# Kernel tuning notes

Hardware: AMD Instinct MI355X
Metric: run time of the kernel (lower is better)

## Reference

```python
import jax, jax.numpy as jnp
import numpy as np


def _bilinear_resample(imgs, dvfs):
    # imgs: (B,H,W,C), dvfs: (B,H,W,2) with channel 0 = x(width) offset, 1 = y(height) offset
    B, H, W, C = imgs.shape
    fx = jnp.arange(W, dtype=imgs.dtype)[None, None, :] + dvfs[..., 0]  # (B,H,W)
    fy = jnp.arange(H, dtype=imgs.dtype)[None, :, None] + dvfs[..., 1]  # (B,H,W)

    x0f = jnp.floor(fx)
    y0f = jnp.floor(fy)
    wx = fx - x0f  # fractional weights
    wy = fy - y0f
    x0 = x0f.astype(jnp.int32)
    y0 = y0f.astype(jnp.int32)
    x1 = x0 + 1
    y1 = y0 + 1

    def gather(iy, ix):
        # zero-padding semantics for out-of-bounds corners (tf resampler behavior)
        valid = (ix >= 0) & (ix < W) & (iy >= 0) & (iy < H)
        ixc = jnp.clip(ix, 0, W - 1)
        iyc = jnp.clip(iy, 0, H - 1)
        vals = jax.vmap(lambda im, yy, xx: im[yy, xx])(imgs, iyc, ixc)  # (B,H,W,C)
        return vals * valid[..., None].astype(imgs.dtype)

    v00 = gather(y0, x0)
    v01 = gather(y0, x1)
    v10 = gather(y1, x0)
    v11 = gather(y1, x1)

    wx = wx[..., None]
    wy = wy[..., None]
    return (v00 * (1 - wx) * (1 - wy)
            + v01 * wx * (1 - wy)
            + v10 * (1 - wx) * wy
            + v11 * wx * wy)


def setup_inputs() -> dict:
    key = jax.random.key(0)
    k1, k2 = jax.random.split(key)
    B, H, W = 32, 1024, 1024
    imgs = jax.random.normal(k1, (B, H, W, 1), dtype=jnp.float32)
    dvfs = jax.random.normal(k2, (B, H, W, 2), dtype=jnp.float32)
    return {"imgs": imgs, "dvfs": dvfs}


def reference(imgs, dvfs):
    return _bilinear_resample(imgs, dvfs)
```

## Files before the change

kernel.cpp:

```cpp
#include <hip/hip_runtime.h>


#define H_DIM 1024
#define W_DIM 1024
#define HW_SHIFT 20
#define HW_PIX (1 << HW_SHIFT)

__device__ __forceinline__ float gather_zp(const float* __restrict__ img,
                                           int yy, int xx) {
    bool valid = (xx >= 0) & (xx < W_DIM) & (yy >= 0) & (yy < H_DIM);
    int xc = min(max(xx, 0), W_DIM - 1);
    int yc = min(max(yy, 0), H_DIM - 1);
    float v = img[yc * W_DIM + xc];
    return valid ? v : 0.0f;
}

__global__ __launch_bounds__(256) void bilerp_kernel(
        const float* __restrict__ imgs,
        const float* __restrict__ dvfs,
        float* __restrict__ out,
        int total_pixels) {
    int pix = blockIdx.x * 256 + threadIdx.x;
    if (pix >= total_pixels) return;

    int b   = pix >> HW_SHIFT;
    int rem = pix & (HW_PIX - 1);
    int y   = rem >> 10;
    int x   = rem & (W_DIM - 1);

    const float* __restrict__ img = imgs + ((long long)b << HW_SHIFT);

    union { double d64; float2 f2; } cvt;
    cvt.d64 = __builtin_nontemporal_load(
        reinterpret_cast<const double*>(dvfs) + pix);
    float dx = cvt.f2.x;
    float dy = cvt.f2.y;

    float fx = (float)x + dx;
    float fy = (float)y + dy;
    float x0f = floorf(fx);
    float y0f = floorf(fy);
    float wx = fx - x0f;
    float wy = fy - y0f;
    int x0 = (int)x0f;
    int y0 = (int)y0f;

    float v00 = gather_zp(img, y0,     x0);
    float v01 = gather_zp(img, y0,     x0 + 1);
    float v10 = gather_zp(img, y0 + 1, x0);
    float v11 = gather_zp(img, y0 + 1, x0 + 1);

    float res = v00 * (1.0f - wx) * (1.0f - wy)
              + v01 * wx          * (1.0f - wy)
              + v10 * (1.0f - wx) * wy
              + v11 * wx          * wy;

    __builtin_nontemporal_store(res, out + pix);
}

extern "C" void kernel_launch(void* const* d_in, const int* in_sizes, int n_in,
                              void* d_out, int out_size, void* d_ws, size_t ws_size,
                              hipStream_t stream) {
    const float* imgs = (const float*)d_in[0];
    const float* dvfs = (const float*)d_in[1];
    float* out = (float*)d_out;

    int total_pixels = out_size;
    int block = 256;
    int grid = (total_pixels + block - 1) / block;

    bilerp_kernel<<<grid, block, 0, stream>>>(imgs, dvfs, out, total_pixels);
}
```

Before: 505.9 us.

## Stage image tiles with halo in shared memory for bilinear gathers

Each block now processes a 64x64 output tile per batch image, first loading a 81x81 halo region of the source image into LDS. Bilinear corner lookups read from LDS when the sampled point falls inside the halo, and fall back to global gathers otherwise. The aim is to replace scattered global/L2 gathers with LDS reads. In exchange it adds a synchronization barrier, about 1.6x redundant image loading because of the halo, and lower occupancy from the LDS footprint.

```diff
diff --git a/kernel.cpp b/kernel.cpp
--- a/kernel.cpp
+++ b/kernel.cpp
@@ -4,7 +4,9 @@
 #define H_DIM 1024
 #define W_DIM 1024
 #define HW_SHIFT 20
-#define HW_PIX (1 << HW_SHIFT)
+#define TILE 64
+#define HALO 8
+#define S_DIM (TILE + 2 * HALO + 1)
 
 __device__ __forceinline__ float gather_zp(const float* __restrict__ img,
                                            int yy, int xx) {
@@ -18,44 +20,81 @@
 __global__ __launch_bounds__(256) void bilerp_kernel(
         const float* __restrict__ imgs,
         const float* __restrict__ dvfs,
-        float* __restrict__ out,
-        int total_pixels) {
-    int pix = blockIdx.x * 256 + threadIdx.x;
-    if (pix >= total_pixels) return;
+        float* __restrict__ out) {
+    __shared__ float tile[S_DIM * S_DIM];
 
-    int b   = pix >> HW_SHIFT;
-    int rem = pix & (HW_PIX - 1);
-    int y   = rem >> 10;
-    int x   = rem & (W_DIM - 1);
+    const int gx0 = blockIdx.x * TILE;
+    const int gy0 = blockIdx.y * TILE;
+    const int b   = blockIdx.z;
+    const int tid = threadIdx.x;
 
     const float* __restrict__ img = imgs + ((long long)b << HW_SHIFT);
 
-    union { double d64; float2 f2; } cvt;
-    cvt.d64 = __builtin_nontemporal_load(
-        reinterpret_cast<const double*>(dvfs) + pix);
-    float dx = cvt.f2.x;
-    float dy = cvt.f2.y;
+    const int x_base = gx0 - HALO;
+    const int y_base = gy0 - HALO;
+    for (int idx = tid; idx < S_DIM * S_DIM; idx += 256) {
+        int r = idx / S_DIM;
+        int c = idx - r * S_DIM;
+        int gy = y_base + r;
+        int gx = x_base + c;
+        float v = 0.0f;
+        if ((unsigned)gy < (unsigned)H_DIM && (unsigned)gx < (unsigned)W_DIM)
+            v = img[(gy << 10) + gx];
+        tile[idx] = v;
+    }
+    __syncthreads();
 
-    float fx = (float)x + dx;
-    float fy = (float)y + dy;
-    float x0f = floorf(fx);
-    float y0f = floorf(fy);
-    float wx = fx - x0f;
-    float wy = fy - y0f;
-    int x0 = (int)x0f;
-    int y0 = (int)y0f;
+    const int tx = tid & 63;
+    const int ty = tid >> 6;
+    const float* __restrict__ dv_img =
+        dvfs + (((long long)b << HW_SHIFT) << 1);
+    float* __restrict__ out_img = out + ((long long)b << HW_SHIFT);
 
-    float v00 = gather_zp(img, y0,     x0);
-    float v01 = gather_zp(img, y0,     x0 + 1);
-    float v10 = gather_zp(img, y0 + 1, x0);
-    float v11 = gather_zp(img, y0 + 1, x0 + 1);
+    for (int i = 0; i < 16; ++i) {
+        int y = gy0 + (i << 2) + ty;
+        int x = gx0 + tx;
+        int pix = (y << 10) + x;
 
-    float res = v00 * (1.0f - wx) * (1.0f - wy)
-              + v01 * wx          * (1.0f - wy)
-              + v10 * (1.0f - wx) * wy
-              + v11 * wx          * wy;
+        union { double d64; float2 f2; } cvt;
+        cvt.d64 = __builtin_nontemporal_load(
+            reinterpret_cast<const double*>(dv_img) + pix);
+        float dx = cvt.f2.x;
+        float dy = cvt.f2.y;
 
-    __builtin_nontemporal_store(res, out + pix);
+        float fx = (float)x + dx;
+        float fy = (float)y + dy;
+        float x0f = floorf(fx);
+        float y0f = floorf(fy);
+        float wx = fx - x0f;
+        float wy = fy - y0f;
+        int x0 = (int)x0f;
+        int y0 = (int)y0f;
+
+        int lx = x0 - x_base;
+        int ly = y0 - y_base;
+
+        float v00, v01, v10, v11;
+        if ((unsigned)lx < (unsigned)(S_DIM - 1) &&
+            (unsigned)ly < (unsigned)(S_DIM - 1)) {
+            const float* p = &tile[ly * S_DIM + lx];
+            v00 = p[0];
+            v01 = p[1];
+            v10 = p[S_DIM];
+            v11 = p[S_DIM + 1];
+        } else {
+            v00 = gather_zp(img, y0,     x0);
+            v01 = gather_zp(img, y0,     x0 + 1);
+            v10 = gather_zp(img, y0 + 1, x0);
+            v11 = gather_zp(img, y0 + 1, x0 + 1);
+        }
+
+        float res = v00 * (1.0f - wx) * (1.0f - wy)
+                  + v01 * wx          * (1.0f - wy)
+                  + v10 * (1.0f - wx) * wy
+                  + v11 * wx          * wy;
+
+        __builtin_nontemporal_store(res, out_img + pix);
+    }
 }
 
 extern "C" void kernel_launch(void* const* d_in, const int* in_sizes, int n_in,
@@ -65,9 +104,6 @@
     const float* dvfs = (const float*)d_in[1];
     float* out = (float*)d_out;
 
-    int total_pixels = out_size;
-    int block = 256;
-    int grid = (total_pixels + block - 1) / block;
-
-    bilerp_kernel<<<grid, block, 0, stream>>>(imgs, dvfs, out, total_pixels);
+    dim3 grid(W_DIM / TILE, H_DIM / TILE, 32);
+    bilerp_kernel<<<grid, 256, 0, stream>>>(imgs, dvfs, out);
 }
```

Measured after the change: 527.7 us. +4.3%, slower.
